# Kernel tuning notes

Hardware: AMD Instinct MI355X
Metric: run time of the kernel (lower is better)

## Reference

```python
import jax, jax.numpy as jnp
import numpy as np

B, D, T = 16, 512, 2048
H = 2
HD = D // H

def setup_inputs() -> dict:
    key = jax.random.key(0)
    k1, k2, k3, k4 = jax.random.split(key, 4)
    s_in = 1.0 / np.sqrt(D)   # torch default-like uniform init for weight_matrix
    s_t = 1.0 / np.sqrt(T)    # nn.Linear default init bound
    xs = jax.random.normal(k1, (B, D, T), dtype=jnp.float32)
    W_KQ = jax.random.uniform(k2, (D, D), jnp.float32, -s_in, s_in)
    W_PV = jax.random.uniform(k3, (D, D), jnp.float32, -s_in, s_in)
    W_out = jax.random.uniform(k4, (T, T), jnp.float32, -s_t, s_t)
    return {"xs": xs, "W_KQ": W_KQ, "W_PV": W_PV, "W_out": W_out}

def reference(xs, W_KQ, W_PV, W_out):
    b, d, t = xs.shape
    xs_skip = xs[:, :, :-1]                                   # [B, D, T-1]
    # xskq = xs_skip^T @ W_KQ  -> [B, T-1, D]
    xskq = jnp.einsum('bds,dj->bsj', xs_skip, W_KQ)
    # split heads: [B, H, T-1, HD]
    xskq_split = xskq.reshape(b, t - 1, H, HD).transpose(0, 2, 1, 3)
    # xs reshaped to heads along feature dim: [B, H, HD, T]
    xs_r = xs.reshape(b, H, HD, t)
    attn_arg = jnp.matmul(xskq_split, xs_r)                   # [B, H, T-1, T], rho=1
    # NON-STANDARD: softmax over the head axis (size 2)
    sm = jax.nn.softmax(attn_arg, axis=1)
    # W_PV @ xs_skip -> [B, D, T-1], split into heads [B, H, HD, T-1]
    wpvx = jnp.einsum('id,bds->bis', W_PV, xs_skip).reshape(b, H, HD, t - 1)
    f_attn = jnp.matmul(wpvx, sm).reshape(b, d, t)            # [B, D, T]
    # output = Linear(T, T, bias=None) then take last token:
    # out[b, i] = sum_t f_attn[b, i, t] * W_out[T-1, t]
    out = jnp.einsum('bdt,t->bd', f_attn, W_out[-1])
    return out
```

## Files before the change

### kernel.cpp

```cpp
#include <hip/hip_runtime.h>
#include <hip/hip_bf16.h>

#define NB 16
#define ND 512
#define NT 2048
#define TM1 2047
#define NHD 256

typedef __attribute__((ext_vector_type(8))) short bf16x8;
typedef __attribute__((ext_vector_type(4))) float f32x4;
typedef unsigned short ushort_t;
typedef unsigned int uint_t;

#define G0_OFF    0ull
#define G0_ELEMS  (16ull * 2047ull)
#define R0_OFF    32768ull
#define SX_OFF    40960ull
#define ZERO_FLOATS 49152ull
#define WSUM_OFF  49152ull
#define WKQT_OFF  49408ull
#define CHUNK_OFF 180480ull
#define BATCH_US  (2048ull * 512ull)
#define BATCH_FLOATS (2ull * 524288ull)

__device__ __forceinline__ ushort_t f2bf(float x) {
    union { float f; uint_t u; } v; v.f = x;
    uint_t r = v.u + 0x7FFFu + ((v.u >> 16) & 1u);
    return (ushort_t)(r >> 16);
}
__device__ __forceinline__ float bf2f(uint_t u) {
    union { uint_t u; float f; } v; v.u = u << 16;
    return v.f;
}

__device__ __forceinline__ void async_copy16(const ushort_t* g, ushort_t* l) {
    __builtin_amdgcn_global_load_lds(
        (const __attribute__((address_space(1))) void*)g,
        (__attribute__((address_space(3))) void*)l, 16, 0, 0);
}

#define FENCE() asm volatile("" ::: "memory")
#define BARRIER() do { FENCE(); __builtin_amdgcn_s_barrier(); FENCE(); } while (0)
#define WAITVM4() asm volatile("s_waitcnt vmcnt(4)" ::: "memory")
#define WAITVM0() asm volatile("s_waitcnt vmcnt(0)" ::: "memory")

__global__ __launch_bounds__(256) void k_cvt_xst(const float* __restrict__ xs,
                                                 ushort_t* __restrict__ xst, int b0,
                                                 const float* __restrict__ wkq,
                                                 ushort_t* __restrict__ wkqT,
                                                 const float* __restrict__ wlast,
                                                 float* __restrict__ wsum,
                                                 float* __restrict__ zbase) {
    __shared__ float tile[64][257];
    const int t0 = blockIdx.x * 256, d0 = blockIdx.y * 64;
    const int cc = blockIdx.z;
    const float* xb = xs + (size_t)(b0 + cc) * ND * NT;
    ushort_t* xo = xst + (size_t)cc * BATCH_US;
    const int wave = threadIdx.x >> 6, lane = threadIdx.x & 63;
    #pragma unroll
    for (int i = 0; i < 16; ++i) {
        const int row = wave * 16 + i;
        *(float4*)&tile[row][lane * 4] =
            *(const float4*)&xb[(size_t)(d0 + row) * NT + t0 + lane * 4];
    }
    __syncthreads();
    const int c8 = (threadIdx.x & 7) * 8;
    #pragma unroll
    for (int i = 0; i < 8; ++i) {
        const int t = i * 32 + (threadIdx.x >> 3);
        uint_t w[4];
        #pragma unroll
        for (int p = 0; p < 4; ++p)
            w[p] = (uint_t)f2bf(tile[c8 + 2 * p][t]) |
                   ((uint_t)f2bf(tile[c8 + 2 * p + 1][t]) << 16);
        *(uint4*)&xo[(size_t)(t0 + t) * ND + d0 + c8] = *(uint4*)w;
    }
    if (cc == 0 && b0 == 0) {
        __shared__ float ptile[32][33];
        const int bid = blockIdx.y * 8 + blockIdx.x;
        const int c = threadIdx.x & 31, r = threadIdx.x >> 5;
        #pragma unroll 1
        for (int q = 0; q < 4; ++q) {
            const int job = bid * 4 + q;
            const int j0 = (job & 15) * 32, dd0 = (job >> 4) * 32;
            __syncthreads();
            #pragma unroll
            for (int i = 0; i < 4; ++i)
                ptile[r + i * 8][c] = wkq[(size_t)(dd0 + r + i * 8) * ND + j0 + c];
            __syncthreads();
            #pragma unroll
            for (int i = 0; i < 4; ++i)
                wkqT[(size_t)(j0 + r + i * 8) * ND + dd0 + c] = f2bf(ptile[c][r + i * 8]);
        }
        #pragma unroll
        for (int k = 0; k < 3; ++k)
            zbase[bid * 768 + k * 256 + threadIdx.x] = 0.f;
        if (bid == 0) {
            __shared__ float red[256];
            float s = 0.f;
            for (int t = threadIdx.x; t < NT; t += 256) s += wlast[t];
            red[threadIdx.x] = s;
            __syncthreads();
            for (int off = 128; off > 0; off >>= 1) {
                if (threadIdx.x < off) red[threadIdx.x] += red[threadIdx.x + off];
                __syncthreads();
            }
            if (threadIdx.x == 0) *wsum = red[0];
        }
    }
}

__device__ __forceinline__ void ld_frag4(bf16x8 (&dst)[4][2], const ushort_t* buf,
                                         int rbase, int l15, int quad, int swz) {
    #pragma unroll
    for (int i = 0; i < 4; ++i)
        #pragma unroll
        for (int kc = 0; kc < 2; ++kc)
            dst[i][kc] = *(const bf16x8*)&buf[(rbase + i * 16 + l15) * 64 + (((kc * 4 + quad) ^ swz) << 3)];
}
__device__ __forceinline__ void ld_frag2(bf16x8 (&dst)[2][2], const ushort_t* buf,
                                         int rbase, int l15, int quad, int swz) {
    #pragma unroll
    for (int i = 0; i < 2; ++i)
        #pragma unroll
        for (int kc = 0; kc < 2; ++kc)
            dst[i][kc] = *(const bf16x8*)&buf[(rbase + i * 16 + l15) * 64 + (((kc * 4 + quad) ^ swz) << 3)];
}
__device__ __forceinline__ void mfma8(f32x4 (&acc)[8][4], const bf16x8 (&a)[4][2],
                                      const bf16x8 (&bb)[2][2], int mbase, int nbase) {
    __builtin_amdgcn_s_setprio(1);
    #pragma unroll
    for (int kc = 0; kc < 2; ++kc)
        #pragma unroll
        for (int mi = 0; mi < 4; ++mi)
            #pragma unroll
            for (int nj = 0; nj < 2; ++nj)
                acc[mbase + mi][nbase + nj] = __builtin_amdgcn_mfma_f32_16x16x32_bf16(
                    a[mi][kc], bb[nj][kc], acc[mbase + mi][nbase + nj], 0, 0, 0);
    __builtin_amdgcn_s_setprio(0);
}

__device__ __forceinline__ void gemm8ph(const ushort_t* __restrict__ Ag,
                                        const ushort_t* __restrict__ Bg,
                                        ushort_t* __restrict__ smA0, ushort_t* __restrict__ smA1,
                                        ushort_t* __restrict__ smB0, ushort_t* __restrict__ smB1,
                                        f32x4 (&acc)[8][4]) {
    const int tid = threadIdx.x;
    const int wave = tid >> 6, lane = tid & 63;
    const int l15 = lane & 15, quad = lane >> 4;
    const int wm = wave >> 2;
    const int swz = l15 & 7;
    const int lrow = lane >> 3;
    const size_t lsrc = (size_t)lrow * ND + (size_t)(((lane & 7) ^ lrow) << 3);
    ushort_t* smA[2] = {smA0, smA1};
    ushort_t* smB[2] = {smB0, smB1};

#define STAGE(gb_, buf_, kt_, h_) do {                                        \
        const ushort_t* g_ = (gb_) + (size_t)((h_) * 128 + wave * 8) * ND +   \
                             (kt_) * 64 + lsrc;                               \
        ushort_t* l_ = (buf_) + (h_) * 8192 + wave * 512;                     \
        async_copy16(g_, l_);                                                 \
        async_copy16(g_ + (size_t)64 * ND, l_ + 4096);                        \
    } while (0)

    bf16x8 a[4][2], br[2][2][2];

    STAGE(Bg, smB[0], 0, 0); STAGE(Bg, smB[0], 0, 1);
    STAGE(Ag, smA[0], 0, 0); STAGE(Ag, smA[0], 0, 1);
    STAGE(Bg, smB[1], 1, 0); STAGE(Bg, smB[1], 1, 1);
    WAITVM4();
    BARRIER();

    #pragma unroll
    for (int j = 0; j < 4; ++j) {
        const int kO = 2 * j + 1;
        ld_frag4(a, smA[0], wm * 128, l15, quad, swz);
        ld_frag2(br[0], smB[0], (wave & 3) * 64, l15, quad, swz);
        STAGE(Ag, smA[1], kO, 0);
        BARRIER();
        mfma8(acc, a, br[0], 0, 0);
        BARRIER();
        ld_frag2(br[1], smB[0], (wave & 3) * 64 + 32, l15, quad, swz);
        STAGE(Ag, smA[1], kO, 1);
        BARRIER();
        mfma8(acc, a, br[1], 0, 2);
        BARRIER();
        ld_frag4(a, smA[0], wm * 128 + 64, l15, quad, swz);
        if (j < 3) STAGE(Bg, smB[0], 2 * j + 2, 0);
        BARRIER();
        mfma8(acc, a, br[0], 4, 0);
        BARRIER();
        if (j < 3) STAGE(Bg, smB[0], 2 * j + 2, 1);
        BARRIER();
        mfma8(acc, a, br[1], 4, 2);
        if (j < 3) { WAITVM4(); } else { WAITVM0(); }
        BARRIER();
        ld_frag4(a, smA[1], wm * 128, l15, quad, swz);
        ld_frag2(br[0], smB[1], (wave & 3) * 64, l15, quad, swz);
        if (j < 3) STAGE(Ag, smA[0], 2 * j + 2, 0);
        BARRIER();
        mfma8(acc, a, br[0], 0, 0);
        BARRIER();
        ld_frag2(br[1], smB[1], (wave & 3) * 64 + 32, l15, quad, swz);
        if (j < 3) STAGE(Ag, smA[0], 2 * j + 2, 1);
        BARRIER();
        mfma8(acc, a, br[1], 0, 2);
        BARRIER();
        ld_frag4(a, smA[1], wm * 128 + 64, l15, quad, swz);
        if (j < 3) STAGE(Bg, smB[1], kO + 2, 0);
        BARRIER();
        mfma8(acc, a, br[0], 4, 0);
        BARRIER();
        if (j < 3) STAGE(Bg, smB[1], kO + 2, 1);
        BARRIER();
        mfma8(acc, a, br[1], 4, 2);
        if (j < 3) WAITVM4();
        BARRIER();
    }
#undef STAGE
}

__global__ __launch_bounds__(512, 2) void k_qd(const ushort_t* __restrict__ xst,
                                               const ushort_t* __restrict__ wkqT,
                                               ushort_t* __restrict__ qdb) {
    __shared__ __align__(16) ushort_t smA[2][16384];
    __shared__ __align__(16) ushort_t smB[2][16384];
    const int lin = blockIdx.x + gridDim.x * (blockIdx.y + gridDim.y * blockIdx.z);
    const int nwg8 = (gridDim.x * gridDim.y * gridDim.z) >> 3;
    const int logical = (lin & 7) * nwg8 + (lin >> 3);
    const int jt = logical & 1;
    const int st = (logical >> 1) & 7;
    const int cc = logical >> 4;
    const int j0 = jt * 256, s0 = st * 256;

    const ushort_t* Ag = xst + (size_t)cc * BATCH_US + (size_t)s0 * ND;
    const ushort_t* Bg = wkqT + (size_t)j0 * ND;
    ushort_t* qo = qdb + (size_t)cc * BATCH_US;

    f32x4 acc[8][4];
    #pragma unroll
    for (int mi = 0; mi < 8; ++mi)
        #pragma unroll
        for (int nj = 0; nj < 4; ++nj) acc[mi][nj] = (f32x4){0.f, 0.f, 0.f, 0.f};

    gemm8ph(Ag, Bg, smA[0], smA[1], smB[0], smB[1], acc);

    const int tid = threadIdx.x;
    const int wave = tid >> 6, lane = tid & 63;
    const int l15 = lane & 15, quad = lane >> 4;
    const int wm = wave >> 2, wn = wave & 3;
    const float sgn = (j0 == 0) ? 1.f : -1.f;
    #pragma unroll
    for (int mi = 0; mi < 8; ++mi) {
        const int srow = s0 + wm * 128 + mi * 16 + quad * 4;
        #pragma unroll
        for (int nj = 0; nj < 4; ++nj) {
            const int jcol = j0 + wn * 64 + nj * 16 + l15;
            #pragma unroll
            for (int r = 0; r < 4; ++r)
                qo[(size_t)(srow + r) * ND + jcol] = f2bf(sgn * acc[mi][nj][r]);
        }
    }
}

__global__ __launch_bounds__(256, 2) void k_attn(const ushort_t* __restrict__ qdb,
                                                 const ushort_t* __restrict__ xst,
                                                 const float* __restrict__ wlast,
                                                 float* __restrict__ g0, int b0) {
    __shared__ __align__(16) ushort_t smA0[8192], smA1[8192];
    __shared__ __align__(16) ushort_t smB0[8192], smB1[8192];
    __shared__ float lds_g[128];
    const int lin = blockIdx.x + gridDim.x * (blockIdx.y + gridDim.y * blockIdx.z);
    const int nwg8 = (gridDim.x * gridDim.y * gridDim.z) >> 3;
    const int logical = (lin & 7) * nwg8 + (lin >> 3);
    const int st = logical & 15;
    const int th = (logical >> 4) & 1;
    const int cc = logical >> 5;
    const int s0 = st * 128;
    const int b = b0 + cc;

    const int tid = threadIdx.x;
    const int wave = tid >> 6, lane = tid & 63;
    const int l15 = lane & 15, quad = lane >> 4;
    const int wm = wave >> 1, wn = wave & 1;
    const int swz = l15 & 7;
    const int lrow = lane >> 3;
    const size_t lsrc = (size_t)lrow * ND + (size_t)(((lane & 7) ^ lrow) << 3);
    const ushort_t* Ag = qdb + (size_t)cc * BATCH_US + (size_t)s0 * ND;
    const ushort_t* Bg = xst + (size_t)cc * BATCH_US + (size_t)(th * 1024) * ND;

#define STAGEA(dst_, kt_) do {                                                \
        const size_t ko_ = (size_t)(kt_) * 64;                                \
        _Pragma("unroll")                                                     \
        for (int n_ = 0; n_ < 4; ++n_) {                                      \
            const int rb_ = wave * 32 + n_ * 8;                               \
            async_copy16(Ag + (size_t)rb_ * ND + ko_ + lsrc, (dst_) + rb_ * 64); \
        }                                                                     \
    } while (0)
#define STAGEB(dst_, kt_, tt_) do {                                           \
        const size_t ko_ = (size_t)(kt_) * 64;                                \
        const size_t ro_ = (size_t)(tt_) * 128;                               \
        _Pragma("unroll")                                                     \
        for (int n_ = 0; n_ < 4; ++n_) {                                      \
            const int rb_ = wave * 32 + n_ * 8;                               \
            async_copy16(Bg + (ro_ + rb_) * ND + ko_ + lsrc, (dst_) + rb_ * 64); \
        }                                                                     \
    } while (0)
#define COMPUTE(A_, B_) do {                                                  \
        _Pragma("unroll")                                                     \
        for (int kc = 0; kc < 2; ++kc) {                                      \
            bf16x8 af_[4], bf_[4];                                            \
            _Pragma("unroll")                                                 \
            for (int mi = 0; mi < 4; ++mi)                                    \
                af_[mi] = *(const bf16x8*)&(A_)[(wm * 64 + mi * 16 + l15) * 64 \
                          + (((kc * 4 + quad) ^ swz) << 3)];                  \
            _Pragma("unroll")                                                 \
            for (int nj = 0; nj < 4; ++nj)                                    \
                bf_[nj] = *(const bf16x8*)&(B_)[(wn * 64 + nj * 16 + l15) * 64 \
                          + (((kc * 4 + quad) ^ swz) << 3)];                  \
            __builtin_amdgcn_s_setprio(1);                                    \
            _Pragma("unroll")                                                 \
            for (int mi = 0; mi < 4; ++mi)                                    \
                _Pragma("unroll")                                             \
                for (int nj = 0; nj < 4; ++nj)                                \
                    acc[mi][nj] = __builtin_amdgcn_mfma_f32_16x16x32_bf16(    \
                        af_[mi], bf_[nj], acc[mi][nj], 0, 0, 0);              \
            __builtin_amdgcn_s_setprio(0);                                    \
        }                                                                     \
    } while (0)

    f32x4 acc[4][4];
    #pragma unroll
    for (int mi = 0; mi < 4; ++mi)
        #pragma unroll
        for (int nj = 0; nj < 4; ++nj) acc[mi][nj] = (f32x4){0.f, 0.f, 0.f, 0.f};
    if (tid < 128) lds_g[tid] = 0.f;
    __syncthreads();

    STAGEA(smA0, 0);
    STAGEB(smB0, 0, 0);
    WAITVM0();
    BARRIER();

    #pragma unroll 1
    for (int jj = 0; jj < 32; ++jj) {
        const int it1 = 2 * jj + 1, it2 = 2 * jj + 2;
        STAGEA(smA1, it1 & 7);
        STAGEB(smB1, it1 & 7, it1 >> 3);
        COMPUTE(smA0, smB0);
        WAITVM0();
        BARRIER();
        if (jj < 31) {
            STAGEA(smA0, it2 & 7);
            STAGEB(smB0, it2 & 7, it2 >> 3);
        }
        COMPUTE(smA1, smB1);
        if ((jj & 3) == 3) {
            const int tb = th * 1024 + (jj >> 2) * 128;
            float wt[4];
            #pragma unroll
            for (int nj = 0; nj < 4; ++nj) wt[nj] = wlast[tb + wn * 64 + nj * 16 + l15];
            #pragma unroll
            for (int mi = 0; mi < 4; ++mi)
                #pragma unroll
                for (int r = 0; r < 4; ++r) {
                    float v = 0.f;
                    #pragma unroll
                    for (int nj = 0; nj < 4; ++nj) {
                        const float e = __expf(-acc[mi][nj][r]);
                        v = fmaf(__builtin_amdgcn_rcpf(1.f + e), wt[nj], v);
                    }
                    v += __shfl_xor(v, 1);
                    v += __shfl_xor(v, 2);
                    v += __shfl_xor(v, 4);
                    v += __shfl_xor(v, 8);
                    if (l15 == 0) atomicAdd(&lds_g[wm * 64 + mi * 16 + quad * 4 + r], v);
                }
            #pragma unroll
            for (int mi = 0; mi < 4; ++mi)
                #pragma unroll
                for (int nj = 0; nj < 4; ++nj) acc[mi][nj] = (f32x4){0.f, 0.f, 0.f, 0.f};
        }
        WAITVM0();
        BARRIER();
    }
#undef STAGEA
#undef STAGEB
#undef COMPUTE

    __syncthreads();
    if (tid < 128) {
        const int srow = s0 + tid;
        if (srow < TM1) atomicAdd(&g0[b * TM1 + srow], lds_g[tid]);
    }
}

__global__ __launch_bounds__(256) void k_r(const ushort_t* __restrict__ xst,
                                           const float* __restrict__ g0,
                                           float* __restrict__ r0acc,
                                           float* __restrict__ sxacc, int b0) {
    const int sc = blockIdx.x;
    const int cc = blockIdx.y;
    const int b = b0 + cc;
    const ushort_t* xa = xst + (size_t)cc * BATCH_US;
    const float* g = g0 + b * TM1;
    const int d2 = threadIdx.x;
    float a00 = 0.f, a01 = 0.f, a10 = 0.f, a11 = 0.f;
    const int send = (sc == 31) ? 63 : 64;
    for (int si = 0; si < send; ++si) {
        const int s = sc * 64 + si;
        const float gv = g[s];
        const uint_t pk = *(const uint_t*)&xa[(size_t)s * ND + d2 * 2];
        const float x0 = bf2f(pk & 0xFFFFu);
        const float x1 = bf2f(pk >> 16);
        a00 = fmaf(x0, gv, a00); a01 = fmaf(x1, gv, a01);
        a10 += x0; a11 += x1;
    }
    atomicAdd(&r0acc[b * ND + d2 * 2], a00);
    atomicAdd(&r0acc[b * ND + d2 * 2 + 1], a01);
    atomicAdd(&sxacc[b * ND + d2 * 2], a10);
    atomicAdd(&sxacc[b * ND + d2 * 2 + 1], a11);
}

__global__ __launch_bounds__(256) void k_out(const float* __restrict__ wpv,
                                             const float* __restrict__ r0acc,
                                             const float* __restrict__ sxacc,
                                             const float* __restrict__ wsum,
                                             float* __restrict__ out) {
    const int b = blockIdx.x;
    const int i0 = blockIdx.y * 256;
    __shared__ float rs[1024];
    const float wsv = *wsum;
    for (int i = threadIdx.x; i < ND; i += 256) {
        const float r0 = r0acc[b * ND + i];
        const float sx = sxacc[b * ND + i];
        rs[i] = r0;
        rs[ND + i] = fmaf(wsv, sx, -r0);
    }
    __syncthreads();
    const int i = i0 + threadIdx.x;
    const float* wrow = wpv + (size_t)i * ND;
    const float* rh = rs + (i >> 8) * ND;
    float acc = 0.f;
    for (int dd = 0; dd < ND; dd += 4) {
        const float4 wv = *(const float4*)(wrow + dd);
        acc += wv.x * rh[dd] + wv.y * rh[dd + 1] + wv.z * rh[dd + 2] + wv.w * rh[dd + 3];
    }
    out[b * ND + i] = acc;
}

extern "C" void kernel_launch(void* const* d_in, const int* in_sizes, int n_in,
                              void* d_out, int out_size, void* d_ws, size_t ws_size,
                              hipStream_t stream) {
    (void)in_sizes; (void)n_in; (void)out_size;
    const float* xs   = (const float*)d_in[0];
    const float* wkq  = (const float*)d_in[1];
    const float* wpv  = (const float*)d_in[2];
    const float* wout = (const float*)d_in[3];
    const float* wlast = wout + (size_t)(NT - 1) * NT;

    float* ws    = (float*)d_ws;
    float* g0    = ws + G0_OFF;
    float* r0acc = ws + R0_OFF;
    float* sxacc = ws + SX_OFF;
    float* wsum  = ws + WSUM_OFF;
    ushort_t* wkqT = (ushort_t*)(ws + WKQT_OFF);

    const size_t ws_floats = ws_size / 4;
    size_t avail = (ws_floats > CHUNK_OFF) ? (ws_floats - CHUNK_OFF) : 0;
    int C = (int)(avail / BATCH_FLOATS);
    if (C > NB) C = NB;
    if (C < 1) C = 1;
    ushort_t* qdb = (ushort_t*)(ws + CHUNK_OFF);
    ushort_t* xst = (ushort_t*)(ws + CHUNK_OFF + (size_t)C * 524288ull);

    for (int b0 = 0; b0 < NB; b0 += C) {
        const int cb = (NB - b0 < C) ? (NB - b0) : C;
        k_cvt_xst<<<dim3(8, 8, cb), 256, 0, stream>>>(xs, xst, b0,
                                                      wkq, wkqT, wlast, wsum, ws);
        k_qd     <<<dim3(2, 8, cb),  512, 0, stream>>>(xst, wkqT, qdb);
        k_attn   <<<dim3(16, 2, cb), 256, 0, stream>>>(qdb, xst, wlast, g0, b0);
        k_r      <<<dim3(32, cb),    256, 0, stream>>>(xst, g0, r0acc, sxacc, b0);
    }
    k_out<<<dim3(NB, 2), 256, 0, stream>>>(wpv, r0acc, sxacc, wsum, (float*)d_out);
}
```

Baseline: 269.5 us.

## Single-buffer k_attn LDS and split T into quarters for higher occupancy

The attention kernel drops LDS double buffering, going from four 16 KB buffers to two, and raises launch bounds to 4 blocks per CU. The T dimension is now split into four 512-column quarters instead of two halves, doubling the grid so there are more, shorter workgroups. The goal is to hide latency through occupancy rather than software prefetch, at the cost of exposing load latency within each block (load, wait, barrier, compute) and adding more g0 atomics.

```diff
diff --git a/kernel.cpp b/kernel.cpp
--- a/kernel.cpp
+++ b/kernel.cpp
@@ -13,10 +13,8 @@
 typedef unsigned int uint_t;
 
 #define G0_OFF    0ull
-#define G0_ELEMS  (16ull * 2047ull)
 #define R0_OFF    32768ull
 #define SX_OFF    40960ull
-#define ZERO_FLOATS 49152ull
 #define WSUM_OFF  49152ull
 #define WKQT_OFF  49408ull
 #define CHUNK_OFF 180480ull
@@ -263,19 +261,19 @@
     }
 }
 
-__global__ __launch_bounds__(256, 2) void k_attn(const ushort_t* __restrict__ qdb,
+__global__ __launch_bounds__(256, 4) void k_attn(const ushort_t* __restrict__ qdb,
                                                  const ushort_t* __restrict__ xst,
                                                  const float* __restrict__ wlast,
                                                  float* __restrict__ g0, int b0) {
-    __shared__ __align__(16) ushort_t smA0[8192], smA1[8192];
-    __shared__ __align__(16) ushort_t smB0[8192], smB1[8192];
+    __shared__ __align__(16) ushort_t smA[8192];
+    __shared__ __align__(16) ushort_t smB[8192];
     __shared__ float lds_g[128];
     const int lin = blockIdx.x + gridDim.x * (blockIdx.y + gridDim.y * blockIdx.z);
     const int nwg8 = (gridDim.x * gridDim.y * gridDim.z) >> 3;
     const int logical = (lin & 7) * nwg8 + (lin >> 3);
     const int st = logical & 15;
-    const int th = (logical >> 4) & 1;
-    const int cc = logical >> 5;
+    const int tq = (logical >> 4) & 3;
+    const int cc = logical >> 6;
     const int s0 = st * 128;
     const int b = b0 + cc;
 
@@ -287,36 +285,36 @@
     const int lrow = lane >> 3;
     const size_t lsrc = (size_t)lrow * ND + (size_t)(((lane & 7) ^ lrow) << 3);
     const ushort_t* Ag = qdb + (size_t)cc * BATCH_US + (size_t)s0 * ND;
-    const ushort_t* Bg = xst + (size_t)cc * BATCH_US + (size_t)(th * 1024) * ND;
-
-#define STAGEA(dst_, kt_) do {                                                \
+    const ushort_t* Bg = xst + (size_t)cc * BATCH_US + (size_t)(tq * 512) * ND;
+
+#define STAGEA(kt_) do {                                                      \
         const size_t ko_ = (size_t)(kt_) * 64;                                \
         _Pragma("unroll")                                                     \
         for (int n_ = 0; n_ < 4; ++n_) {                                      \
             const int rb_ = wave * 32 + n_ * 8;                               \
-            async_copy16(Ag + (size_t)rb_ * ND + ko_ + lsrc, (dst_) + rb_ * 64); \
+            async_copy16(Ag + (size_t)rb_ * ND + ko_ + lsrc, smA + rb_ * 64); \
         }                                                                     \
     } while (0)
-#define STAGEB(dst_, kt_, tt_) do {                                           \
+#define STAGEB(kt_, tt_) do {                                                 \
         const size_t ko_ = (size_t)(kt_) * 64;                                \
         const size_t ro_ = (size_t)(tt_) * 128;                               \
         _Pragma("unroll")                                                     \
         for (int n_ = 0; n_ < 4; ++n_) {                                      \
             const int rb_ = wave * 32 + n_ * 8;                               \
-            async_copy16(Bg + (ro_ + rb_) * ND + ko_ + lsrc, (dst_) + rb_ * 64); \
+            async_copy16(Bg + (ro_ + rb_) * ND + ko_ + lsrc, smB + rb_ * 64); \
         }                                                                     \
     } while (0)
-#define COMPUTE(A_, B_) do {                                                  \
+#define COMPUTE() do {                                                        \
         _Pragma("unroll")                                                     \
         for (int kc = 0; kc < 2; ++kc) {                                      \
             bf16x8 af_[4], bf_[4];                                            \
             _Pragma("unroll")                                                 \
             for (int mi = 0; mi < 4; ++mi)                                    \
-                af_[mi] = *(const bf16x8*)&(A_)[(wm * 64 + mi * 16 + l15) * 64 \
+                af_[mi] = *(const bf16x8*)&smA[(wm * 64 + mi * 16 + l15) * 64 \
                           + (((kc * 4 + quad) ^ swz) << 3)];                  \
             _Pragma("unroll")                                                 \
             for (int nj = 0; nj < 4; ++nj)                                    \
-                bf_[nj] = *(const bf16x8*)&(B_)[(wn * 64 + nj * 16 + l15) * 64 \
+                bf_[nj] = *(const bf16x8*)&smB[(wn * 64 + nj * 16 + l15) * 64 \
                           + (((kc * 4 + quad) ^ swz) << 3)];                  \
             __builtin_amdgcn_s_setprio(1);                                    \
             _Pragma("unroll")                                                 \
@@ -335,28 +333,17 @@
         #pragma unroll
         for (int nj = 0; nj < 4; ++nj) acc[mi][nj] = (f32x4){0.f, 0.f, 0.f, 0.f};
     if (tid < 128) lds_g[tid] = 0.f;
-    __syncthreads();
-
-    STAGEA(smA0, 0);
-    STAGEB(smB0, 0, 0);
-    WAITVM0();
-    BARRIER();
 
     #pragma unroll 1
-    for (int jj = 0; jj < 32; ++jj) {
-        const int it1 = 2 * jj + 1, it2 = 2 * jj + 2;
-        STAGEA(smA1, it1 & 7);
-        STAGEB(smB1, it1 & 7, it1 >> 3);
-        COMPUTE(smA0, smB0);
+    for (int it = 0; it < 32; ++it) {
+        const int kt = it & 7, tt = it >> 3;
+        STAGEA(kt);
+        STAGEB(kt, tt);
         WAITVM0();
         BARRIER();
-        if (jj < 31) {
-            STAGEA(smA0, it2 & 7);
-            STAGEB(smB0, it2 & 7, it2 >> 3);
-        }
-        COMPUTE(smA1, smB1);
-        if ((jj & 3) == 3) {
-            const int tb = th * 1024 + (jj >> 2) * 128;
+        COMPUTE();
+        if (kt == 7) {
+            const int tb = tq * 512 + tt * 128;
             float wt[4];
             #pragma unroll
             for (int nj = 0; nj < 4; ++nj) wt[nj] = wlast[tb + wn * 64 + nj * 16 + l15];
@@ -381,7 +368,6 @@
                 #pragma unroll
                 for (int nj = 0; nj < 4; ++nj) acc[mi][nj] = (f32x4){0.f, 0.f, 0.f, 0.f};
         }
-        WAITVM0();
         BARRIER();
     }
 #undef STAGEA
@@ -479,7 +465,7 @@
         k_cvt_xst<<<dim3(8, 8, cb), 256, 0, stream>>>(xs, xst, b0,
                                                       wkq, wkqT, wlast, wsum, ws);
         k_qd     <<<dim3(2, 8, cb),  512, 0, stream>>>(xst, wkqT, qdb);
-        k_attn   <<<dim3(16, 2, cb), 256, 0, stream>>>(qdb, xst, wlast, g0, b0);
+        k_attn   <<<dim3(16, 4, cb), 256, 0, stream>>>(qdb, xst, wlast, g0, b0);
         k_r      <<<dim3(32, cb),    256, 0, stream>>>(xst, g0, r0acc, sxacc, b0);
     }
     k_out<<<dim3(NB, 2), 256, 0, stream>>>(wpv, r0acc, sxacc, wsum, (float*)d_out);
```

After: 261.0 us. 3.1% less time.
